# Kernel optimization log

Hardware: AMD Instinct MI355X
Metric: run time of the kernel (lower is better)

Reference implementation:

```python
import jax, jax.numpy as jnp
import numpy as np

B, NL, NH, CL, CH = 16, 4096, 1024, 128, 256
MLP = [256, 256]
BN_EPS = 1e-5


def setup_inputs() -> dict:
    key = jax.random.key(0)
    ks = jax.random.split(key, 8)
    inp = {
        "xyz_low": jax.random.normal(ks[0], (B, NL, 3), dtype=jnp.float32),
        "xyz_high": jax.random.normal(ks[1], (B, NH, 3), dtype=jnp.float32),
        "feat_low": jax.random.normal(ks[2], (B, CL, NL), dtype=jnp.float32),
        "feat_high": jax.random.normal(ks[3], (B, CH, NH), dtype=jnp.float32),
    }
    last = CL + CH
    for i, oc in enumerate(MLP):
        inp[f"W{i}"] = jax.random.normal(ks[4 + i], (oc, last), dtype=jnp.float32) * (1.0 / np.sqrt(last))
        inp[f"b{i}"] = jnp.zeros((oc,), dtype=jnp.float32)
        inp[f"gamma{i}"] = jnp.ones((oc,), dtype=jnp.float32)
        inp[f"beta{i}"] = jnp.zeros((oc,), dtype=jnp.float32)
        last = oc
    return inp


def _bn_relu(x, gamma, beta):
    # BatchNorm1d in training mode: batch stats over (B, N) per channel (biased var)
    mean = x.mean(axis=(0, 2), keepdims=True)
    var = ((x - mean) ** 2).mean(axis=(0, 2), keepdims=True)
    y = gamma[None, :, None] * (x - mean) * jax.lax.rsqrt(var + BN_EPS) + beta[None, :, None]
    return jax.nn.relu(y)


def _forward(xyz_low, xyz_high, feat_low, feat_high,
             W0, b0, gamma0, beta0, W1, b1, gamma1, beta1):
    # pairwise euclidean distances (B, NL, NH)
    d2 = (jnp.sum(xyz_low ** 2, -1)[:, :, None]
          + jnp.sum(xyz_high ** 2, -1)[:, None, :]
          - 2.0 * jnp.einsum('bnd,bmd->bnm', xyz_low, xyz_high))
    d = jnp.sqrt(jnp.maximum(d2, 0.0))
    # 3 nearest neighbours (smallest distances)
    _, idx = jax.lax.top_k(-d, 3)                       # (B, NL, 3)
    dist = jnp.maximum(jnp.take_along_axis(d, idx, axis=-1), 1e-8)
    w = 1.0 / dist
    w = w / w.sum(axis=-1, keepdims=True)               # (B, NL, 3)
    fT = jnp.swapaxes(feat_high, 1, 2)                  # (B, NH, CH)
    neigh = jax.vmap(lambda f, i: f[i])(fT, idx)        # (B, NL, 3, CH)
    f_interp = jnp.einsum('bnk,bnkc->bcn', w, neigh)    # (B, CH, NL)
    x = jnp.concatenate([f_interp, feat_low], axis=1)   # (B, CL+CH, NL)
    # 1x1 Conv -> BN -> ReLU stack
    x = _bn_relu(jnp.einsum('bcn,oc->bon', x, W0) + b0[None, :, None], gamma0, beta0)
    x = _bn_relu(jnp.einsum('bcn,oc->bon', x, W1) + b1[None, :, None], gamma1, beta1)
    return x


def reference(xyz_low, xyz_high, feat_low, feat_high,
              W0, b0, gamma0, beta0, W1, b1, gamma1, beta1):
    return _forward(xyz_low, xyz_high, feat_low, feat_high,
                    W0, b0, gamma0, beta0, W1, b1, gamma1, beta1)
```

## Files before the change

kernel.cpp:

```cpp
#include <hip/hip_runtime.h>
#include <math.h>

#define BB 16
#define NL 4096
#define NH 1024
#define CL 128
#define CHH 256
#define K0 384
#define K1 256
#define CO 256
#define BN_EPS 1e-5f

typedef __attribute__((ext_vector_type(8))) short bfrag;
typedef __attribute__((ext_vector_type(4))) float f32x4;
typedef __attribute__((ext_vector_type(4))) unsigned short ushort4b;

__device__ inline unsigned short f2bf(float f) {
    unsigned int u = __builtin_bit_cast(unsigned int, f);
    u += 0x7fffu + ((u >> 16) & 1u);
    return (unsigned short)(u >> 16);
}
__device__ inline float bf2f(unsigned short h) {
    unsigned int u = ((unsigned int)h) << 16;
    return __builtin_bit_cast(float, u);
}

__global__ __launch_bounds__(256) void k_setup(const float* __restrict__ W0s,
                                               unsigned short* __restrict__ Wb0,
                                               const float* __restrict__ W1s,
                                               unsigned short* __restrict__ Wb1,
                                               const float* __restrict__ xyzh,
                                               float4* __restrict__ cand4) {
    int i = blockIdx.x * 256 + threadIdx.x;
    if (i < CO * K0) Wb0[i] = f2bf(W0s[i]);
    if (i < CO * K1) Wb1[i] = f2bf(W1s[i]);
    if (i < BB * NH) {
        float x = xyzh[3 * i], y = xyzh[3 * i + 1], z = xyzh[3 * i + 2];
        float ss = __fadd_rn(__fadd_rn(__fmul_rn(x, x), __fmul_rn(y, y)),
                             __fmul_rn(z, z));
        cand4[i] = make_float4(x, y, z, ss);
    }
}

__global__ __launch_bounds__(256) void k_transpose_fh(const float* __restrict__ fh,
                                                      unsigned short* __restrict__ fT) {
    __shared__ float s[32][33];
    int b = blockIdx.z;
    int c0 = blockIdx.y * 32;
    int m0 = blockIdx.x * 32;
    int tx = threadIdx.x % 32, ty = threadIdx.x / 32;
    const float* src = fh + (size_t)b * CHH * NH;
    unsigned short* dst = fT + (size_t)b * NH * CHH;
#pragma unroll
    for (int j = 0; j < 4; j++)
        s[ty + 8 * j][tx] = src[(size_t)(c0 + ty + 8 * j) * NH + m0 + tx];
    __syncthreads();
    int mi = threadIdx.x >> 3;
    int cp = threadIdx.x & 7;
#pragma unroll
    for (int h = 0; h < 2; h++) {
        int ci = (cp + 8 * h) * 2;
        unsigned int o = (unsigned int)f2bf(s[ci][mi]) |
                         ((unsigned int)f2bf(s[ci + 1][mi]) << 16);
        *(unsigned int*)&dst[(size_t)(m0 + mi) * CHH + c0 + ci] = o;
    }
}

__global__ __launch_bounds__(256) void k_knn(const float* __restrict__ xyzl,
                                             const float4* __restrict__ cand4,
                                             int* __restrict__ idx,
                                             float* __restrict__ wgt) {
    __shared__ float4 cnd[NH];
    __shared__ float tls[4][64][3];
    __shared__ int   ils[4][64][3];

    int b = blockIdx.y;
    for (int p = threadIdx.x; p < NH; p += 256)
        cnd[p] = cand4[(size_t)b * NH + p];
    __syncthreads();

    int lane = threadIdx.x & 63;
    int w = threadIdx.x >> 6;
    int n = blockIdx.x * 64 + lane;

    const float* xl = xyzl + ((size_t)b * NL + n) * 3;
    float l0 = xl[0], l1 = xl[1], l2 = xl[2];
    float a = __fadd_rn(__fadd_rn(__fmul_rn(l0, l0), __fmul_rn(l1, l1)),
                        __fmul_rn(l2, l2));

    float t0 = INFINITY, t1 = INFINITY, t2 = INFINITY;
    int i0 = 0, i1 = 0, i2 = 0;
    int mb = w * 256;
#pragma unroll 8
    for (int j = 0; j < 256; j++) {
        float4 c = cnd[mb + j];
        int m = mb + j;
        float dot = __fadd_rn(__fadd_rn(__fmul_rn(l0, c.x), __fmul_rn(l1, c.y)),
                              __fmul_rn(l2, c.z));
        float dd = __fsub_rn(__fadd_rn(a, c.w), __fmul_rn(2.0f, dot));
        bool c0 = dd < t0, c1 = dd < t1, c2 = dd < t2;
        float nt0 = fminf(dd, t0);
        float nt1 = __builtin_amdgcn_fmed3f(dd, t0, t1);
        float nt2 = __builtin_amdgcn_fmed3f(dd, t1, t2);
        i2 = c1 ? i1 : (c2 ? m : i2);
        i1 = c0 ? i0 : (c1 ? m : i1);
        i0 = c0 ? m : i0;
        t0 = nt0; t1 = nt1; t2 = nt2;
    }
    tls[w][lane][0] = t0; tls[w][lane][1] = t1; tls[w][lane][2] = t2;
    ils[w][lane][0] = i0; ils[w][lane][1] = i1; ils[w][lane][2] = i2;
    __syncthreads();

    if (threadIdx.x < 64) {
        int p = threadIdx.x;
        float u0 = tls[0][p][0], u1 = tls[0][p][1], u2 = tls[0][p][2];
        int   j0 = ils[0][p][0], j1 = ils[0][p][1], j2 = ils[0][p][2];
#pragma unroll
        for (int sg = 1; sg < 4; sg++) {
#pragma unroll
            for (int e = 0; e < 3; e++) {
                float dd = tls[sg][p][e];
                int m = ils[sg][p][e];
                bool c0 = dd < u0, c1 = dd < u1, c2 = dd < u2;
                u2 = c1 ? u1 : (c2 ? dd : u2);
                j2 = c1 ? j1 : (c2 ? m : j2);
                u1 = c0 ? u0 : (c1 ? dd : u1);
                j1 = c0 ? j0 : (c1 ? m : j1);
                u0 = c0 ? dd : u0;
                j0 = c0 ? m : j0;
            }
        }
        u0 = fmaxf(u0, 0.0f); u1 = fmaxf(u1, 0.0f); u2 = fmaxf(u2, 0.0f);
        float d0 = sqrtf(u0), d1 = sqrtf(u1), d2 = sqrtf(u2);
        float w0 = 1.0f / fmaxf(d0, 1e-8f);
        float w1 = 1.0f / fmaxf(d1, 1e-8f);
        float w2 = 1.0f / fmaxf(d2, 1e-8f);
        float wsum = __fadd_rn(__fadd_rn(w0, w1), w2);
        w0 /= wsum; w1 /= wsum; w2 /= wsum;
        int nn = blockIdx.x * 64 + p;
        size_t base = ((size_t)b * NL + nn) * 3;
        idx[base] = j0; idx[base + 1] = j1; idx[base + 2] = j2;
        wgt[base] = w0; wgt[base + 1] = w1; wgt[base + 2] = w2;
    }
}

__global__ __launch_bounds__(256) void k_fl_t(const float* __restrict__ fl,
                                              unsigned short* __restrict__ Xb2) {
    __shared__ unsigned short s[32][68];
    int b = blockIdx.z, c0 = blockIdx.y * 32, n0 = blockIdx.x * 64;
    int tx = threadIdx.x & 63, ty = threadIdx.x >> 6;
    const float* src = fl + ((size_t)b * CL + c0) * NL + n0;
#pragma unroll
    for (int i = 0; i < 8; i++) {
        int c = ty * 8 + i;
        s[c][tx] = f2bf(src[(size_t)c * NL + tx]);
    }
    __syncthreads();
    int n = threadIdx.x >> 2, q = threadIdx.x & 3;
    ushort4b o0, o1;
#pragma unroll
    for (int e = 0; e < 4; e++) o0[e] = s[q * 8 + e][n];
#pragma unroll
    for (int e = 0; e < 4; e++) o1[e] = s[q * 8 + 4 + e][n];
    unsigned short* dst = Xb2 + ((size_t)b * NL + n0 + n) * CL + c0 + q * 8;
    *(ushort4b*)dst = o0;
    *(ushort4b*)(dst + 4) = o1;
}

__device__ inline bfrag bnrelu8(bfrag v, f32x4 s0, f32x4 s1, f32x4 h0, f32x4 h1) {
    bfrag o;
#pragma unroll
    for (int e = 0; e < 4; e++)
        o[e] = (short)f2bf(fmaxf(fmaf(s0[e], bf2f((unsigned short)v[e]), h0[e]), 0.f));
#pragma unroll
    for (int e = 0; e < 4; e++)
        o[4 + e] = (short)f2bf(fmaxf(fmaf(s1[e], bf2f((unsigned short)v[4 + e]), h1[e]), 0.f));
    return o;
}

__device__ inline bfrag interp8(bfrag f0, bfrag f1, bfrag f2,
                                float w0, float w1, float w2) {
    bfrag o;
#pragma unroll
    for (int e = 0; e < 8; e++) {
        float f = __fadd_rn(__fadd_rn(__fmul_rn(w0, bf2f((unsigned short)f0[e])),
                                      __fmul_rn(w1, bf2f((unsigned short)f1[e]))),
                            __fmul_rn(w2, bf2f((unsigned short)f2[e])));
        o[e] = (short)f2bf(f);
    }
    return o;
}

__device__ inline int swz(int r, int cb) {
    return r * 32 + ((cb ^ ((r >> 1) & 3)) << 3);
}

#define EROW 264

template <int K, bool INTERP, bool BN>
__global__ __launch_bounds__(512) void k_gemmf(const unsigned short* __restrict__ X,
                                               const unsigned short* __restrict__ fT,
                                               const int* __restrict__ idx,
                                               const float* __restrict__ wgt,
                                               const unsigned short* __restrict__ Wb,
                                               const float* __restrict__ bias,
                                               const float* __restrict__ bnsc,
                                               const float* __restrict__ bnsh,
                                               unsigned short* __restrict__ Y,
                                               float* __restrict__ psumT,
                                               float* __restrict__ psqT) {
    __shared__ __align__(16) unsigned short smem[2 * 256 * 32 + 2 * 128 * 32];
    unsigned short (*sA)[256 * 32] = (unsigned short (*)[256 * 32])smem;
    unsigned short (*sB)[128 * 32] = (unsigned short (*)[128 * 32])(smem + 2 * 256 * 32);
    unsigned short* sE = smem;

    int bt = blockIdx.x;
    int xcd = bt & 7, ii = bt >> 3;
    int b  = xcd * 2 + (ii >> 5);
    int n0 = (ii & 31) * 128;

    int tid = threadIdx.x;
    int lane = tid & 63;
    int wid = tid >> 6;
    int wm = wid >> 1, wn = wid & 1;

    int sr = tid >> 2;
    int scb = tid & 3;
    int swA0 = swz(sr, scb), swA1 = swz(sr + 128, scb);
    int swB = swz(sr, scb);

    const unsigned short* Wt = Wb + scb * 8;
    int nrow = n0 + sr;

    const unsigned short* fTb;
    int ba0 = 0, ba1 = 0, ba2 = 0;
    float iw0 = 0.f, iw1 = 0.f, iw2 = 0.f;
    if (INTERP) {
        size_t ib = ((size_t)b * NL + nrow) * 3;
        ba0 = idx[ib] * CHH; ba1 = idx[ib + 1] * CHH; ba2 = idx[ib + 2] * CHH;
        iw0 = wgt[ib]; iw1 = wgt[ib + 1]; iw2 = wgt[ib + 2];
        fTb = fT + (size_t)b * NH * CHH;
    }
    const unsigned short* Xrow =
        X + ((size_t)b * NL + nrow) * (INTERP ? CL : CO);

    f32x4 acc[4][4] = {};

    auto stageB = [&](int tt, bfrag& r0, bfrag& r1, bfrag& r2) {
        int cg = tt * 32 + scb * 8;
        if (INTERP) {
            if (cg < CHH) {
                r0 = *(const bfrag*)&fTb[ba0 + cg];
                r1 = *(const bfrag*)&fTb[ba1 + cg];
                r2 = *(const bfrag*)&fTb[ba2 + cg];
            } else {
                r0 = *(const bfrag*)&Xrow[cg - CHH];
            }
        } else {
            r0 = *(const bfrag*)&Xrow[cg];
        }
    };
    auto combineB = [&](int tt, bfrag r0, bfrag r1, bfrag r2) -> bfrag {
        int cg = tt * 32 + scb * 8;
        if (INTERP) {
            if (cg < CHH) return interp8(r0, r1, r2, iw0, iw1, iw2);
            return r0;
        }
        if (BN) {
            f32x4 sc0 = *(const f32x4*)&bnsc[cg], sc1 = *(const f32x4*)&bnsc[cg + 4];
            f32x4 sh0 = *(const f32x4*)&bnsh[cg], sh1 = *(const f32x4*)&bnsh[cg + 4];
            return bnrelu8(r0, sc0, sc1, sh0, sh1);
        }
        return r0;
    };

    {
        bfrag a0 = *(const bfrag*)&Wt[(size_t)sr * K];
        bfrag a1 = *(const bfrag*)&Wt[(size_t)(sr + 128) * K];
        bfrag r0, r1, r2;
        stageB(0, r0, r1, r2);
        bfrag bb = combineB(0, r0, r1, r2);
        *(bfrag*)&sA[0][swA0] = a0;
        *(bfrag*)&sA[0][swA1] = a1;
        *(bfrag*)&sB[0][swB] = bb;
    }
    __syncthreads();

    const int nkt = K / 32;
    int cur = 0;
#pragma unroll 2
    for (int tt = 0; tt < nkt; tt++) {
        bfrag na0, na1, r0, r1, r2;
        bool more = (tt + 1 < nkt);
        if (more) {
            int kk = (tt + 1) * 32;
            na0 = *(const bfrag*)&Wt[(size_t)sr * K + kk];
            na1 = *(const bfrag*)&Wt[(size_t)(sr + 128) * K + kk];
            stageB(tt + 1, r0, r1, r2);
        }
        bfrag af[4], bf[4];
#pragma unroll
        for (int mi = 0; mi < 4; mi++) {
            int r = wm * 64 + mi * 16 + (lane & 15);
            af[mi] = *(const bfrag*)&sA[cur][swz(r, lane >> 4)];
        }
#pragma unroll
        for (int ni = 0; ni < 4; ni++) {
            int r = wn * 64 + ni * 16 + (lane & 15);
            bf[ni] = *(const bfrag*)&sB[cur][swz(r, lane >> 4)];
        }
#pragma unroll
        for (int mi = 0; mi < 4; mi++)
#pragma unroll
            for (int ni = 0; ni < 4; ni++)
                acc[mi][ni] = __builtin_amdgcn_mfma_f32_16x16x32_bf16(
                    af[mi], bf[ni], acc[mi][ni], 0, 0, 0);
        if (more) {
            bfrag nb = combineB(tt + 1, r0, r1, r2);
            *(bfrag*)&sA[cur ^ 1][swA0] = na0;
            *(bfrag*)&sA[cur ^ 1][swA1] = na1;
            *(bfrag*)&sB[cur ^ 1][swB] = nb;
            __syncthreads();
            cur ^= 1;
        }
    }

    __syncthreads();

    int col = lane & 15, rg = (lane >> 4) << 2;
    int slot = bt * 2 + wn;
#pragma unroll
    for (int mi = 0; mi < 4; mi++) {
        int m = wm * 64 + mi * 16 + rg;
        f32x4 bv = *(const f32x4*)&bias[m];
        f32x4 sacc = {0.f, 0.f, 0.f, 0.f}, qacc = {0.f, 0.f, 0.f, 0.f};
#pragma unroll
        for (int ni = 0; ni < 4; ni++) {
            f32x4 c = acc[mi][ni];
#pragma unroll
            for (int j = 0; j < 4; j++) {
                float sv = c[j] + bv[j];
                sacc[j] += sv;
                qacc[j] += sv * sv;
            }
        }
#pragma unroll
        for (int j = 0; j < 4; j++) {
            float s = sacc[j], q = qacc[j];
#pragma unroll
            for (int off = 1; off < 16; off <<= 1) {
                s += __shfl_xor(s, off, 64);
                q += __shfl_xor(q, off, 64);
            }
            if (col == 0) {
                psumT[(size_t)(m + j) * 1024 + slot] = s;
                psqT[(size_t)(m + j) * 1024 + slot] = q;
            }
        }
    }

#pragma unroll
    for (int half = 0; half < 2; half++) {
        if (wn == half) {
#pragma unroll
            for (int mi = 0; mi < 4; mi++) {
                int m = wm * 64 + mi * 16 + rg;
                f32x4 bv = *(const f32x4*)&bias[m];
#pragma unroll
                for (int ni = 0; ni < 4; ni++) {
                    int nloc = ni * 16 + col;
                    f32x4 c = acc[mi][ni];
                    ushort4b o;
                    o[0] = f2bf(c[0] + bv[0]); o[1] = f2bf(c[1] + bv[1]);
                    o[2] = f2bf(c[2] + bv[2]); o[3] = f2bf(c[3] + bv[3]);
                    *(ushort4b*)&sE[nloc * EROW + m] = o;
                }
            }
        }
        __syncthreads();
#pragma unroll
        for (int s2 = 0; s2 < 4; s2++) {
            int row = s2 * 16 + (tid >> 5);
            int ch = tid & 31;
            *(bfrag*)&Y[((size_t)b * NL + n0 + half * 64 + row) * CO + ch * 8] =
                *(const bfrag*)&sE[row * EROW + ch * 8];
        }
        __syncthreads();
    }
}

__global__ __launch_bounds__(256) void k_fin(const float* __restrict__ psumT,
                                             const float* __restrict__ psqT,
                                             const float* __restrict__ gamma,
                                             const float* __restrict__ beta,
                                             float* __restrict__ scale,
                                             float* __restrict__ shift) {
    int c = blockIdx.x;
    const float* ps = psumT + (size_t)c * 1024;
    const float* pq = psqT + (size_t)c * 1024;
    float s = 0.f, q = 0.f;
    for (int i = threadIdx.x; i < 1024; i += 256) { s += ps[i]; q += pq[i]; }
#pragma unroll
    for (int off = 1; off < 64; off <<= 1) {
        s += __shfl_xor(s, off, 64);
        q += __shfl_xor(q, off, 64);
    }
    __shared__ float ls[4], lq[4];
    if ((threadIdx.x & 63) == 0) { ls[threadIdx.x >> 6] = s; lq[threadIdx.x >> 6] = q; }
    __syncthreads();
    if (threadIdx.x == 0) {
        float S = ls[0] + ls[1] + ls[2] + ls[3];
        float Q = lq[0] + lq[1] + lq[2] + lq[3];
        float N = (float)(BB * NL);
        float mean = S / N;
        float var = Q / N - mean * mean;
        float sc = gamma[c] / sqrtf(var + BN_EPS);
        scale[c] = sc;
        shift[c] = beta[c] - mean * sc;
    }
}

__global__ __launch_bounds__(256) void k_out(const unsigned short* __restrict__ y1,
                                             const float* __restrict__ scale,
                                             const float* __restrict__ shift,
                                             float* __restrict__ out) {
    __shared__ float s[64][65];
    int b = blockIdx.z, m0 = blockIdx.y * 64, n0 = blockIdx.x * 64;
    int r = threadIdx.x >> 3;
    int mq = (threadIdx.x & 7) * 8;
#pragma unroll
    for (int it = 0; it < 2; it++) {
        int row = r + it * 32;
        bfrag v = *(const bfrag*)&y1[((size_t)b * NL + n0 + row) * CO + m0 + mq];
#pragma unroll
        for (int e = 0; e < 8; e++) {
            int m = mq + e;
            float f = bf2f((unsigned short)v[e]);
            s[m][row] = fmaxf(fmaf(scale[m0 + m], f, shift[m0 + m]), 0.f);
        }
    }
    __syncthreads();
    int ch = threadIdx.x & 15;
    int mb4 = threadIdx.x >> 4;
#pragma unroll
    for (int it = 0; it < 4; it++) {
        int m = it * 16 + mb4;
        float4 v = make_float4(s[m][ch * 4], s[m][ch * 4 + 1],
                               s[m][ch * 4 + 2], s[m][ch * 4 + 3]);
        *(float4*)&out[((size_t)b * CO + m0 + m) * NL + n0 + ch * 4] = v;
    }
}

extern "C" void kernel_launch(void* const* d_in, const int* in_sizes, int n_in,
                              void* d_out, int out_size, void* d_ws, size_t ws_size,
                              hipStream_t stream) {
    const float* xyz_low   = (const float*)d_in[0];
    const float* xyz_high  = (const float*)d_in[1];
    const float* feat_low  = (const float*)d_in[2];
    const float* feat_high = (const float*)d_in[3];
    const float* W0  = (const float*)d_in[4];
    const float* b0  = (const float*)d_in[5];
    const float* g0  = (const float*)d_in[6];
    const float* be0 = (const float*)d_in[7];
    const float* W1  = (const float*)d_in[8];
    const float* b1  = (const float*)d_in[9];
    const float* g1  = (const float*)d_in[10];
    const float* be1 = (const float*)d_in[11];
    float* out = (float*)d_out;

    char* ws = (char*)d_ws;
    unsigned short* Xb2 = (unsigned short*)ws;
    unsigned short* y0  = (unsigned short*)(ws + ((size_t)16 << 20));
    unsigned short* y1  = (unsigned short*)(ws + ((size_t)48 << 20));
    unsigned short* fT  = (unsigned short*)(ws + ((size_t)48 << 20));
    char* tail          = ws + ((size_t)80 << 20);
    int*    idx   = (int*)tail;
    float*  wgt   = (float*)(tail + 786432);
    float4* cand4 = (float4*)(tail + 2 * 786432);
    unsigned short* Wb0 = (unsigned short*)(tail + 2 * 786432 + 262144);
    unsigned short* Wb1 = Wb0 + CO * K0;
    char* tail2   = (char*)(Wb1 + CO * K1);
    float* psumT0 = (float*)tail2;
    float* psqT0  = psumT0 + 256 * 1024;
    float* psumT1 = psqT0 + 256 * 1024;
    float* psqT1  = psumT1 + 256 * 1024;
    float* prm    = psqT1 + 256 * 1024;
    float* scale0 = prm,        *shift0 = prm + 256;
    float* scale1 = prm + 512,  *shift1 = prm + 768;

    k_setup<<<(CO * K0 + 255) / 256, 256, 0, stream>>>(W0, Wb0, W1, Wb1,
                                                       xyz_high, cand4);
    k_transpose_fh<<<dim3(NH / 32, CHH / 32, BB), 256, 0, stream>>>(feat_high, fT);
    k_knn<<<dim3(NL / 64, BB), 256, 0, stream>>>(xyz_low, cand4, idx, wgt);
    k_fl_t<<<dim3(NL / 64, CL / 32, BB), 256, 0, stream>>>(feat_low, Xb2);

    k_gemmf<K0, true, false><<<512, 512, 0, stream>>>(
        Xb2, fT, idx, wgt, Wb0, b0, nullptr, nullptr, y0, psumT0, psqT0);
    k_fin<<<256, 256, 0, stream>>>(psumT0, psqT0, g0, be0, scale0, shift0);
    k_gemmf<K1, false, true><<<512, 512, 0, stream>>>(
        y0, nullptr, nullptr, nullptr, Wb1, b1, scale0, shift0, y1, psumT1, psqT1);
    k_fin<<<256, 256, 0, stream>>>(psumT1, psqT1, g1, be1, scale1, shift1);
    k_out<<<dim3(NL / 64, CO / 64, BB), 256, 0, stream>>>(y1, scale1, shift1, out);
}
```

Before: 146.8 us.

## Use direct global-to-LDS double-buffered GEMM for second conv layer

Replaces the second fused GEMM (k_gemmf with 512-thread blocks covering full output channels) with a new k_gemm kernel using 256-thread blocks, 128x128 tiles, and 1024 blocks. Operands stream straight into swizzled LDS via global_load_lds, double-buffered over 32-wide K slices, so the next slice's load overlaps the current slice's MFMAs. BN+ReLU of the previous layer is still applied on the B fragments, and per-tile BN partial sums are written to the same slot layout. The aim is better latency hiding and occupancy, at the cost of redoing the BN transform for each M half and trusting the slot mapping to match k_fin.

Measured after the change: 155.4 us. 1.06x slower.

```diff
diff --git a/kernel.cpp b/kernel.cpp
--- a/kernel.cpp
+++ b/kernel.cpp
@@ -23,6 +23,13 @@
 __device__ inline float bf2f(unsigned short h) {
     unsigned int u = ((unsigned int)h) << 16;
     return __builtin_bit_cast(float, u);
+}
+
+__device__ __forceinline__ void gl_lds16(const unsigned short* g, unsigned short* l) {
+    __builtin_amdgcn_global_load_lds(
+        (const __attribute__((address_space(1))) unsigned int*)(const void*)g,
+        (__attribute__((address_space(3))) unsigned int*)(void*)l,
+        16, 0, 0);
 }
 
 __global__ __launch_bounds__(256) void k_setup(const float* __restrict__ W0s,
@@ -384,6 +391,156 @@
             int ch = tid & 31;
             *(bfrag*)&Y[((size_t)b * NL + n0 + half * 64 + row) * CO + ch * 8] =
                 *(const bfrag*)&sE[row * EROW + ch * 8];
+        }
+        __syncthreads();
+    }
+}
+
+#define EROW1 136
+
+template <int K, bool BN>
+__global__ __launch_bounds__(256) void k_gemm(const unsigned short* __restrict__ X,
+                                              const unsigned short* __restrict__ Wb,
+                                              const float* __restrict__ bias,
+                                              const float* __restrict__ bnsc,
+                                              const float* __restrict__ bnsh,
+                                              unsigned short* __restrict__ Y,
+                                              float* __restrict__ psumT,
+                                              float* __restrict__ psqT) {
+    __shared__ __align__(16) unsigned short smem[4 * 4096];
+    unsigned short* sA = smem;
+    unsigned short* sB = smem + 2 * 4096;
+    unsigned short* sE = smem;
+
+    int t = blockIdx.x;
+    int xcd = t & 7, ii = t >> 3;
+    int m0 = (ii & 1) * 128;
+    int nb = ii >> 1;
+    int n0 = (nb & 31) * 128;
+    int b  = xcd * 2 + (nb >> 5);
+    int slotbase = (xcd * 64 + (t >> 4)) * 2;
+
+    int tid = threadIdx.x;
+    int lane = tid & 63;
+    int w = tid >> 6;
+    int wm = w >> 1, wn = w & 1;
+
+    int srow = w * 32 + (lane >> 2);
+    int schunk = (lane & 3) ^ ((srow >> 1) & 3);
+    const unsigned short* gA0 = Wb + (size_t)(m0 + srow) * K + schunk * 8;
+    const unsigned short* gA1 = Wb + (size_t)(m0 + srow + 16) * K + schunk * 8;
+    const unsigned short* gB0 = X + ((size_t)b * NL + n0 + srow) * K + schunk * 8;
+    const unsigned short* gB1 = X + ((size_t)b * NL + n0 + srow + 16) * K + schunk * 8;
+    unsigned short* lA0 = sA + (w * 32) * 32;
+    unsigned short* lA1 = sA + (w * 32 + 16) * 32;
+    unsigned short* lB0 = sB + (w * 32) * 32;
+    unsigned short* lB1 = sB + (w * 32 + 16) * 32;
+
+    f32x4 acc[4][4] = {};
+
+    gl_lds16(gA0, lA0);
+    gl_lds16(gA1, lA1);
+    gl_lds16(gB0, lB0);
+    gl_lds16(gB1, lB1);
+    __syncthreads();
+
+    const int nkt = K / 32;
+    int cur = 0;
+#pragma unroll 2
+    for (int tt = 0; tt < nkt; tt++) {
+        if (tt + 1 < nkt) {
+            int kk = (tt + 1) * 32;
+            int off = (cur ^ 1) * 4096;
+            gl_lds16(gA0 + kk, lA0 + off);
+            gl_lds16(gA1 + kk, lA1 + off);
+            gl_lds16(gB0 + kk, lB0 + off);
+            gl_lds16(gB1 + kk, lB1 + off);
+        }
+        bfrag af[4], bf[4];
+#pragma unroll
+        for (int mi = 0; mi < 4; mi++) {
+            int r = wm * 64 + mi * 16 + (lane & 15);
+            af[mi] = *(const bfrag*)&sA[cur * 4096 + swz(r, lane >> 4)];
+        }
+#pragma unroll
+        for (int ni = 0; ni < 4; ni++) {
+            int r = wn * 64 + ni * 16 + (lane & 15);
+            bfrag raw = *(const bfrag*)&sB[cur * 4096 + swz(r, lane >> 4)];
+            if (BN) {
+                int cg = tt * 32 + (lane >> 4) * 8;
+                f32x4 sc0 = *(const f32x4*)&bnsc[cg], sc1 = *(const f32x4*)&bnsc[cg + 4];
+                f32x4 sh0 = *(const f32x4*)&bnsh[cg], sh1 = *(const f32x4*)&bnsh[cg + 4];
+                bf[ni] = bnrelu8(raw, sc0, sc1, sh0, sh1);
+            } else {
+                bf[ni] = raw;
+            }
+        }
+#pragma unroll
+        for (int mi = 0; mi < 4; mi++)
+#pragma unroll
+            for (int ni = 0; ni < 4; ni++)
+                acc[mi][ni] = __builtin_amdgcn_mfma_f32_16x16x32_bf16(
+                    af[mi], bf[ni], acc[mi][ni], 0, 0, 0);
+        __syncthreads();
+        cur ^= 1;
+    }
+
+    int col = lane & 15, rg = (lane >> 4) << 2;
+#pragma unroll
+    for (int mi = 0; mi < 4; mi++) {
+        int m = m0 + wm * 64 + mi * 16 + rg;
+        f32x4 bv = *(const f32x4*)&bias[m];
+        f32x4 sacc = {0.f, 0.f, 0.f, 0.f}, qacc = {0.f, 0.f, 0.f, 0.f};
+#pragma unroll
+        for (int ni = 0; ni < 4; ni++) {
+            f32x4 c = acc[mi][ni];
+#pragma unroll
+            for (int j = 0; j < 4; j++) {
+                float sv = c[j] + bv[j];
+                sacc[j] += sv;
+                qacc[j] += sv * sv;
+            }
+        }
+#pragma unroll
+        for (int j = 0; j < 4; j++) {
+            float s = sacc[j], q = qacc[j];
+#pragma unroll
+            for (int off = 1; off < 16; off <<= 1) {
+                s += __shfl_xor(s, off, 64);
+                q += __shfl_xor(q, off, 64);
+            }
+            if (col == 0) {
+                psumT[(size_t)(m + j) * 1024 + slotbase + wn] = s;
+                psqT[(size_t)(m + j) * 1024 + slotbase + wn] = q;
+            }
+        }
+    }
+
+#pragma unroll
+    for (int half = 0; half < 2; half++) {
+        if (wn == half) {
+#pragma unroll
+            for (int mi = 0; mi < 4; mi++) {
+                int ml = wm * 64 + mi * 16 + rg;
+                f32x4 bv = *(const f32x4*)&bias[m0 + ml];
+#pragma unroll
+                for (int ni = 0; ni < 4; ni++) {
+                    int nloc = ni * 16 + col;
+                    f32x4 c = acc[mi][ni];
+                    ushort4b o;
+                    o[0] = f2bf(c[0] + bv[0]); o[1] = f2bf(c[1] + bv[1]);
+                    o[2] = f2bf(c[2] + bv[2]); o[3] = f2bf(c[3] + bv[3]);
+                    *(ushort4b*)&sE[nloc * EROW1 + ml] = o;
+                }
+            }
+        }
+        __syncthreads();
+#pragma unroll
+        for (int s2 = 0; s2 < 4; s2++) {
+            int row = s2 * 16 + (tid >> 4);
+            int ch = tid & 15;
+            *(bfrag*)&Y[((size_t)b * NL + n0 + half * 64 + row) * CO + m0 + ch * 8] =
+                *(const bfrag*)&sE[row * EROW1 + ch * 8];
         }
         __syncthreads();
     }
@@ -497,8 +654,8 @@
     k_gemmf<K0, true, false><<<512, 512, 0, stream>>>(
         Xb2, fT, idx, wgt, Wb0, b0, nullptr, nullptr, y0, psumT0, psqT0);
     k_fin<<<256, 256, 0, stream>>>(psumT0, psqT0, g0, be0, scale0, shift0);
-    k_gemmf<K1, false, true><<<512, 512, 0, stream>>>(
-        y0, nullptr, nullptr, nullptr, Wb1, b1, scale0, shift0, y1, psumT1, psqT1);
+    k_gemm<K1, true><<<1024, 256, 0, stream>>>(
+        y0, Wb1, b1, scale0, shift0, y1, psumT1, psqT1);
     k_fin<<<256, 256, 0, stream>>>(psumT1, psqT1, g1, be1, scale1, shift1);
     k_out<<<dim3(NL / 64, CO / 64, BB), 256, 0, stream>>>(y1, scale1, shift1, out);
 }
```

## Merge front-end setup, transpose, KNN and feature kernels into one launch

Applied to the files above, without the earlier changes.

Four preprocessing kernels (weight conversion plus candidate packing, feat_high transpose, KNN search, feat_low transpose) are combined into a single kernel whose blocks pick their role from the block index. The candidate xyz/norm packing now happens inside each KNN block instead of in a separate pass through global memory. This removes three launches and the dependency gaps between them, and lets the compute-bound KNN blocks overlap with the memory-bound transpose blocks. In exchange, every block reserves the largest shared-memory footprint (the KNN layout), which may lower occupancy for the transpose blocks.

Result: faster. 129.5 us (-11.8%).

```diff
diff --git a/kernel.cpp b/kernel.cpp
--- a/kernel.cpp
+++ b/kernel.cpp
@@ -25,146 +25,167 @@
     return __builtin_bit_cast(float, u);
 }
 
-__global__ __launch_bounds__(256) void k_setup(const float* __restrict__ W0s,
+#define KNN_BLKS   1024
+#define TR_BLKS    4096
+#define FLT_BLKS   4096
+#define CVT_BLKS   384
+
+struct SMknn { float4 cnd[NH]; float tls[4][64][3]; int ils[4][64][3]; };
+struct SMtr  { float s[32][33]; };
+struct SMflt { unsigned short s[32][68]; };
+
+__global__ __launch_bounds__(256) void k_front(const float* __restrict__ xyzl,
+                                               const float* __restrict__ xyzh,
+                                               const float* __restrict__ fh,
+                                               const float* __restrict__ fl,
+                                               const float* __restrict__ W0s,
+                                               const float* __restrict__ W1s,
                                                unsigned short* __restrict__ Wb0,
-                                               const float* __restrict__ W1s,
                                                unsigned short* __restrict__ Wb1,
-                                               const float* __restrict__ xyzh,
-                                               float4* __restrict__ cand4) {
-    int i = blockIdx.x * 256 + threadIdx.x;
-    if (i < CO * K0) Wb0[i] = f2bf(W0s[i]);
-    if (i < CO * K1) Wb1[i] = f2bf(W1s[i]);
-    if (i < BB * NH) {
-        float x = xyzh[3 * i], y = xyzh[3 * i + 1], z = xyzh[3 * i + 2];
-        float ss = __fadd_rn(__fadd_rn(__fmul_rn(x, x), __fmul_rn(y, y)),
-                             __fmul_rn(z, z));
-        cand4[i] = make_float4(x, y, z, ss);
-    }
-}
-
-__global__ __launch_bounds__(256) void k_transpose_fh(const float* __restrict__ fh,
-                                                      unsigned short* __restrict__ fT) {
-    __shared__ float s[32][33];
-    int b = blockIdx.z;
-    int c0 = blockIdx.y * 32;
-    int m0 = blockIdx.x * 32;
-    int tx = threadIdx.x % 32, ty = threadIdx.x / 32;
-    const float* src = fh + (size_t)b * CHH * NH;
-    unsigned short* dst = fT + (size_t)b * NH * CHH;
-#pragma unroll
-    for (int j = 0; j < 4; j++)
-        s[ty + 8 * j][tx] = src[(size_t)(c0 + ty + 8 * j) * NH + m0 + tx];
-    __syncthreads();
-    int mi = threadIdx.x >> 3;
-    int cp = threadIdx.x & 7;
-#pragma unroll
-    for (int h = 0; h < 2; h++) {
-        int ci = (cp + 8 * h) * 2;
-        unsigned int o = (unsigned int)f2bf(s[ci][mi]) |
-                         ((unsigned int)f2bf(s[ci + 1][mi]) << 16);
-        *(unsigned int*)&dst[(size_t)(m0 + mi) * CHH + c0 + ci] = o;
-    }
-}
-
-__global__ __launch_bounds__(256) void k_knn(const float* __restrict__ xyzl,
-                                             const float4* __restrict__ cand4,
-                                             int* __restrict__ idx,
-                                             float* __restrict__ wgt) {
-    __shared__ float4 cnd[NH];
-    __shared__ float tls[4][64][3];
-    __shared__ int   ils[4][64][3];
-
-    int b = blockIdx.y;
-    for (int p = threadIdx.x; p < NH; p += 256)
-        cnd[p] = cand4[(size_t)b * NH + p];
-    __syncthreads();
-
-    int lane = threadIdx.x & 63;
-    int w = threadIdx.x >> 6;
-    int n = blockIdx.x * 64 + lane;
-
-    const float* xl = xyzl + ((size_t)b * NL + n) * 3;
-    float l0 = xl[0], l1 = xl[1], l2 = xl[2];
-    float a = __fadd_rn(__fadd_rn(__fmul_rn(l0, l0), __fmul_rn(l1, l1)),
-                        __fmul_rn(l2, l2));
-
-    float t0 = INFINITY, t1 = INFINITY, t2 = INFINITY;
-    int i0 = 0, i1 = 0, i2 = 0;
-    int mb = w * 256;
+                                               unsigned short* __restrict__ fT,
+                                               unsigned short* __restrict__ Xb2,
+                                               int* __restrict__ idx,
+                                               float* __restrict__ wgt) {
+    __shared__ __align__(16) char smem_raw[sizeof(SMknn)];
+
+    int blk = blockIdx.x;
+
+    if (blk < KNN_BLKS) {
+        SMknn& sm = *(SMknn*)smem_raw;
+        int b = blk >> 6;
+        int nb = blk & 63;
+        const float* xh = xyzh + (size_t)b * NH * 3;
+        for (int p = threadIdx.x; p < NH; p += 256) {
+            const float* xp = xh + 3 * p;
+            float x = xp[0], y = xp[1], z = xp[2];
+            float ss = __fadd_rn(__fadd_rn(__fmul_rn(x, x), __fmul_rn(y, y)),
+                                 __fmul_rn(z, z));
+            sm.cnd[p] = make_float4(x, y, z, ss);
+        }
+        __syncthreads();
+
+        int lane = threadIdx.x & 63;
+        int w = threadIdx.x >> 6;
+        int n = nb * 64 + lane;
+
+        const float* xl = xyzl + ((size_t)b * NL + n) * 3;
+        float l0 = xl[0], l1 = xl[1], l2 = xl[2];
+        float a = __fadd_rn(__fadd_rn(__fmul_rn(l0, l0), __fmul_rn(l1, l1)),
+                            __fmul_rn(l2, l2));
+
+        float t0 = INFINITY, t1 = INFINITY, t2 = INFINITY;
+        int i0 = 0, i1 = 0, i2 = 0;
+        int mb = w * 256;
 #pragma unroll 8
-    for (int j = 0; j < 256; j++) {
-        float4 c = cnd[mb + j];
-        int m = mb + j;
-        float dot = __fadd_rn(__fadd_rn(__fmul_rn(l0, c.x), __fmul_rn(l1, c.y)),
-                              __fmul_rn(l2, c.z));
-        float dd = __fsub_rn(__fadd_rn(a, c.w), __fmul_rn(2.0f, dot));
-        bool c0 = dd < t0, c1 = dd < t1, c2 = dd < t2;
-        float nt0 = fminf(dd, t0);
-        float nt1 = __builtin_amdgcn_fmed3f(dd, t0, t1);
-        float nt2 = __builtin_amdgcn_fmed3f(dd, t1, t2);
-        i2 = c1 ? i1 : (c2 ? m : i2);
-        i1 = c0 ? i0 : (c1 ? m : i1);
-        i0 = c0 ? m : i0;
-        t0 = nt0; t1 = nt1; t2 = nt2;
-    }
-    tls[w][lane][0] = t0; tls[w][lane][1] = t1; tls[w][lane][2] = t2;
-    ils[w][lane][0] = i0; ils[w][lane][1] = i1; ils[w][lane][2] = i2;
-    __syncthreads();
-
-    if (threadIdx.x < 64) {
-        int p = threadIdx.x;
-        float u0 = tls[0][p][0], u1 = tls[0][p][1], u2 = tls[0][p][2];
-        int   j0 = ils[0][p][0], j1 = ils[0][p][1], j2 = ils[0][p][2];
-#pragma unroll
-        for (int sg = 1; sg < 4; sg++) {
-#pragma unroll
-            for (int e = 0; e < 3; e++) {
-                float dd = tls[sg][p][e];
-                int m = ils[sg][p][e];
-                bool c0 = dd < u0, c1 = dd < u1, c2 = dd < u2;
-                u2 = c1 ? u1 : (c2 ? dd : u2);
-                j2 = c1 ? j1 : (c2 ? m : j2);
-                u1 = c0 ? u0 : (c1 ? dd : u1);
-                j1 = c0 ? j0 : (c1 ? m : j1);
-                u0 = c0 ? dd : u0;
-                j0 = c0 ? m : j0;
+        for (int j = 0; j < 256; j++) {
+            float4 c = sm.cnd[mb + j];
+            int m = mb + j;
+            float dot = __fadd_rn(__fadd_rn(__fmul_rn(l0, c.x), __fmul_rn(l1, c.y)),
+                                  __fmul_rn(l2, c.z));
+            float dd = __fsub_rn(__fadd_rn(a, c.w), __fmul_rn(2.0f, dot));
+            bool c0 = dd < t0, c1 = dd < t1, c2 = dd < t2;
+            float nt0 = fminf(dd, t0);
+            float nt1 = __builtin_amdgcn_fmed3f(dd, t0, t1);
+            float nt2 = __builtin_amdgcn_fmed3f(dd, t1, t2);
+            i2 = c1 ? i1 : (c2 ? m : i2);
+            i1 = c0 ? i0 : (c1 ? m : i1);
+            i0 = c0 ? m : i0;
+            t0 = nt0; t1 = nt1; t2 = nt2;
+        }
+        sm.tls[w][lane][0] = t0; sm.tls[w][lane][1] = t1; sm.tls[w][lane][2] = t2;
+        sm.ils[w][lane][0] = i0; sm.ils[w][lane][1] = i1; sm.ils[w][lane][2] = i2;
+        __syncthreads();
+
+        if (threadIdx.x < 64) {
+            int p = threadIdx.x;
+            float u0 = sm.tls[0][p][0], u1 = sm.tls[0][p][1], u2 = sm.tls[0][p][2];
+            int   j0 = sm.ils[0][p][0], j1 = sm.ils[0][p][1], j2 = sm.ils[0][p][2];
+#pragma unroll
+            for (int sg = 1; sg < 4; sg++) {
+#pragma unroll
+                for (int e = 0; e < 3; e++) {
+                    float dd = sm.tls[sg][p][e];
+                    int m = sm.ils[sg][p][e];
+                    bool c0 = dd < u0, c1 = dd < u1, c2 = dd < u2;
+                    u2 = c1 ? u1 : (c2 ? dd : u2);
+                    j2 = c1 ? j1 : (c2 ? m : j2);
+                    u1 = c0 ? u0 : (c1 ? dd : u1);
+                    j1 = c0 ? j0 : (c1 ? m : j1);
+                    u0 = c0 ? dd : u0;
+                    j0 = c0 ? m : j0;
+                }
             }
-        }
-        u0 = fmaxf(u0, 0.0f); u1 = fmaxf(u1, 0.0f); u2 = fmaxf(u2, 0.0f);
-        float d0 = sqrtf(u0), d1 = sqrtf(u1), d2 = sqrtf(u2);
-        float w0 = 1.0f / fmaxf(d0, 1e-8f);
-        float w1 = 1.0f / fmaxf(d1, 1e-8f);
-        float w2 = 1.0f / fmaxf(d2, 1e-8f);
-        float wsum = __fadd_rn(__fadd_rn(w0, w1), w2);
-        w0 /= wsum; w1 /= wsum; w2 /= wsum;
-        int nn = blockIdx.x * 64 + p;
-        size_t base = ((size_t)b * NL + nn) * 3;
-        idx[base] = j0; idx[base + 1] = j1; idx[base + 2] = j2;
-        wgt[base] = w0; wgt[base + 1] = w1; wgt[base + 2] = w2;
-    }
-}
-
-__global__ __launch_bounds__(256) void k_fl_t(const float* __restrict__ fl,
-                                              unsigned short* __restrict__ Xb2) {
-    __shared__ unsigned short s[32][68];
-    int b = blockIdx.z, c0 = blockIdx.y * 32, n0 = blockIdx.x * 64;
-    int tx = threadIdx.x & 63, ty = threadIdx.x >> 6;
-    const float* src = fl + ((size_t)b * CL + c0) * NL + n0;
-#pragma unroll
-    for (int i = 0; i < 8; i++) {
-        int c = ty * 8 + i;
-        s[c][tx] = f2bf(src[(size_t)c * NL + tx]);
-    }
-    __syncthreads();
-    int n = threadIdx.x >> 2, q = threadIdx.x & 3;
-    ushort4b o0, o1;
-#pragma unroll
-    for (int e = 0; e < 4; e++) o0[e] = s[q * 8 + e][n];
-#pragma unroll
-    for (int e = 0; e < 4; e++) o1[e] = s[q * 8 + 4 + e][n];
-    unsigned short* dst = Xb2 + ((size_t)b * NL + n0 + n) * CL + c0 + q * 8;
-    *(ushort4b*)dst = o0;
-    *(ushort4b*)(dst + 4) = o1;
+            u0 = fmaxf(u0, 0.0f); u1 = fmaxf(u1, 0.0f); u2 = fmaxf(u2, 0.0f);
+            float d0 = sqrtf(u0), d1 = sqrtf(u1), d2 = sqrtf(u2);
+            float w0 = 1.0f / fmaxf(d0, 1e-8f);
+            float w1 = 1.0f / fmaxf(d1, 1e-8f);
+            float w2 = 1.0f / fmaxf(d2, 1e-8f);
+            float wsum = __fadd_rn(__fadd_rn(w0, w1), w2);
+            w0 /= wsum; w1 /= wsum; w2 /= wsum;
+            int nn = nb * 64 + p;
+            size_t base = ((size_t)b * NL + nn) * 3;
+            idx[base] = j0; idx[base + 1] = j1; idx[base + 2] = j2;
+            wgt[base] = w0; wgt[base + 1] = w1; wgt[base + 2] = w2;
+        }
+        return;
+    }
+
+    if (blk < KNN_BLKS + TR_BLKS) {
+        SMtr& sm = *(SMtr*)smem_raw;
+        int t = blk - KNN_BLKS;
+        int m0 = (t & 31) * 32;
+        int c0 = ((t >> 5) & 7) * 32;
+        int b  = t >> 8;
+        int tx = threadIdx.x % 32, ty = threadIdx.x / 32;
+        const float* src = fh + (size_t)b * CHH * NH;
+        unsigned short* dst = fT + (size_t)b * NH * CHH;
+#pragma unroll
+        for (int j = 0; j < 4; j++)
+            sm.s[ty + 8 * j][tx] = src[(size_t)(c0 + ty + 8 * j) * NH + m0 + tx];
+        __syncthreads();
+        int mi = threadIdx.x >> 3;
+        int cp = threadIdx.x & 7;
+#pragma unroll
+        for (int h = 0; h < 2; h++) {
+            int ci = (cp + 8 * h) * 2;
+            unsigned int o = (unsigned int)f2bf(sm.s[ci][mi]) |
+                             ((unsigned int)f2bf(sm.s[ci + 1][mi]) << 16);
+            *(unsigned int*)&dst[(size_t)(m0 + mi) * CHH + c0 + ci] = o;
+        }
+        return;
+    }
+
+    if (blk < KNN_BLKS + TR_BLKS + FLT_BLKS) {
+        SMflt& sm = *(SMflt*)smem_raw;
+        int t = blk - (KNN_BLKS + TR_BLKS);
+        int n0 = (t & 63) * 64;
+        int c0 = ((t >> 6) & 3) * 32;
+        int b  = t >> 8;
+        int tx = threadIdx.x & 63, ty = threadIdx.x >> 6;
+        const float* src = fl + ((size_t)b * CL + c0) * NL + n0;
+#pragma unroll
+        for (int i = 0; i < 8; i++) {
+            int c = ty * 8 + i;
+            sm.s[c][tx] = f2bf(src[(size_t)c * NL + tx]);
+        }
+        __syncthreads();
+        int n = threadIdx.x >> 2, q = threadIdx.x & 3;
+        ushort4b o0, o1;
+#pragma unroll
+        for (int e = 0; e < 4; e++) o0[e] = sm.s[q * 8 + e][n];
+#pragma unroll
+        for (int e = 0; e < 4; e++) o1[e] = sm.s[q * 8 + 4 + e][n];
+        unsigned short* dst = Xb2 + ((size_t)b * NL + n0 + n) * CL + c0 + q * 8;
+        *(ushort4b*)dst = o0;
+        *(ushort4b*)(dst + 4) = o1;
+        return;
+    }
+
+    {
+        int i = (blk - (KNN_BLKS + TR_BLKS + FLT_BLKS)) * 256 + threadIdx.x;
+        if (i < CO * K0) Wb0[i] = f2bf(W0s[i]);
+        if (i < CO * K1) Wb1[i] = f2bf(W1s[i]);
+    }
 }
 
 __device__ inline bfrag bnrelu8(bfrag v, f32x4 s0, f32x4 s1, f32x4 h0, f32x4 h1) {
@@ -476,8 +497,7 @@
     char* tail          = ws + ((size_t)80 << 20);
     int*    idx   = (int*)tail;
     float*  wgt   = (float*)(tail + 786432);
-    float4* cand4 = (float4*)(tail + 2 * 786432);
-    unsigned short* Wb0 = (unsigned short*)(tail + 2 * 786432 + 262144);
+    unsigned short* Wb0 = (unsigned short*)(tail + 2 * 786432);
     unsigned short* Wb1 = Wb0 + CO * K0;
     char* tail2   = (char*)(Wb1 + CO * K1);
     float* psumT0 = (float*)tail2;
@@ -488,11 +508,9 @@
     float* scale0 = prm,        *shift0 = prm + 256;
     float* scale1 = prm + 512,  *shift1 = prm + 768;
 
-    k_setup<<<(CO * K0 + 255) / 256, 256, 0, stream>>>(W0, Wb0, W1, Wb1,
-                                                       xyz_high, cand4);
-    k_transpose_fh<<<dim3(NH / 32, CHH / 32, BB), 256, 0, stream>>>(feat_high, fT);
-    k_knn<<<dim3(NL / 64, BB), 256, 0, stream>>>(xyz_low, cand4, idx, wgt);
-    k_fl_t<<<dim3(NL / 64, CL / 32, BB), 256, 0, stream>>>(feat_low, Xb2);
+    k_front<<<KNN_BLKS + TR_BLKS + FLT_BLKS + CVT_BLKS, 256, 0, stream>>>(
+        xyz_low, xyz_high, feat_high, feat_low, W0, W1,
+        Wb0, Wb1, fT, Xb2, idx, wgt);
 
     k_gemmf<K0, true, false><<<512, 512, 0, stream>>>(
         Xb2, fT, idx, wgt, Wb0, b0, nullptr, nullptr, y0, psumT0, psqT0);
```
